# Performance work log

Hardware: AMD Instinct MI355X
Metric: run time of the kernel (lower is better)

Reference implementation:

```python
import jax, jax.numpy as jnp
import numpy as np
from jax import lax

L = 2048      # sentence length
V = 50000     # vocab size
E = 512       # embedding dim
HD = 512      # per-direction hidden (hidden_dim // 2)
H = 1024      # hidden_dim
T = 48        # tagset size
START, STOP = 46, 47
NEG = -10000.0


def setup_inputs() -> dict:
    key = jax.random.key(0)
    ks = iter(jax.random.split(key, 40))
    def n(shape, s=0.1):
        return jax.random.normal(next(ks), shape, dtype=jnp.float32) * s
    inp = {"sentence": jax.random.randint(next(ks), (L,), 0, V, dtype=jnp.int32)}
    inp["embedding"] = n((V, E), 1.0)
    for l, din in ((0, E), (1, H)):
        for d in ("", "r"):
            inp[f"w_ih_l{l}{d}"] = n((4 * HD, din))
            inp[f"w_hh_l{l}{d}"] = n((4 * HD, HD))
            inp[f"b_ih_l{l}{d}"] = n((4 * HD,))
            inp[f"b_hh_l{l}{d}"] = n((4 * HD,))
    inp["h0"] = n((4, HD), 1.0)
    inp["c0"] = n((4, HD), 1.0)
    inp["W_tag"] = n((T, H))
    inp["b_tag"] = n((T,))
    tr = n((T, T), 1.0)
    inp["transitions"] = tr.at[START, :].set(NEG).at[:, STOP].set(NEG)
    return inp


def _lstm_dir(x, w_ih, w_hh, b_ih, b_hh, h, c, reverse):
    # PyTorch LSTM cell, gates ordered (i, f, g, o). x: [L, Din]
    pre = x @ w_ih.T + (b_ih + b_hh)  # [L, 4*HD]
    def step(carry, p):
        h, c = carry
        g = p + h @ w_hh.T
        i, f, gg, o = jnp.split(g, 4)
        i, f, o = jax.nn.sigmoid(i), jax.nn.sigmoid(f), jax.nn.sigmoid(o)
        c = f * c + i * jnp.tanh(gg)
        h = o * jnp.tanh(c)
        return (h, c), h
    _, hs = lax.scan(step, (h, c), pre, reverse=reverse)
    return hs  # [L, HD], time-aligned with input


def _viterbi(feats, transitions):
    # max-plus recurrence over the tagset, vectorized per timestep
    init = jnp.full((T,), NEG, dtype=feats.dtype).at[START].set(0.0)
    def step(fv, feat):
        scores = fv[None, :] + transitions  # [next_tag, prev_tag]
        bp = jnp.argmax(scores, axis=1)
        return jnp.max(scores, axis=1) + feat, bp
    fv, bps = lax.scan(step, init, feats)  # bps: [L, T]
    terminal = fv + transitions[STOP]
    best = jnp.argmax(terminal)
    score = terminal[best]
    def back(tag, bp):
        prev = bp[tag]
        return prev, prev
    _, ys = lax.scan(back, best, bps, reverse=True)
    # ys[0] == START (dropped); path is tags for t = 0..L-1
    path = jnp.concatenate([ys[1:], best[None]])
    return score, path


def reference(sentence, embedding,
              w_ih_l0, w_hh_l0, b_ih_l0, b_hh_l0,
              w_ih_l0r, w_hh_l0r, b_ih_l0r, b_hh_l0r,
              w_ih_l1, w_hh_l1, b_ih_l1, b_hh_l1,
              w_ih_l1r, w_hh_l1r, b_ih_l1r, b_hh_l1r,
              h0, c0, W_tag, b_tag, transitions):
    embeds = embedding[sentence]  # [L, E]
    l0 = jnp.concatenate([
        _lstm_dir(embeds, w_ih_l0, w_hh_l0, b_ih_l0, b_hh_l0, h0[0], c0[0], False),
        _lstm_dir(embeds, w_ih_l0r, w_hh_l0r, b_ih_l0r, b_hh_l0r, h0[1], c0[1], True),
    ], axis=-1)  # [L, H]
    l1 = jnp.concatenate([
        _lstm_dir(l0, w_ih_l1, w_hh_l1, b_ih_l1, b_hh_l1, h0[2], c0[2], False),
        _lstm_dir(l0, w_ih_l1r, w_hh_l1r, b_ih_l1r, b_hh_l1r, h0[3], c0[3], True),
    ], axis=-1)  # [L, H]
    feats = l1 @ W_tag.T + b_tag  # [L, T]
    score, path = _viterbi(feats, transitions)
    return score, path
```

## Files before the change

kernel.cpp:

```cpp
#include <hip/hip_runtime.h>
#include <hip/hip_bf16.h>

#define L_SEQ 2048
#define HDIM 512
#define NGATE4 2048
#define TAGS 48
#define START_TAG 46
#define STOP_TAG 47
#define NWG 32
#define JPW 16

typedef float f32x4 __attribute__((ext_vector_type(4)));

#define BM 64
#define BN 64
#define BK 32
#define LDT 68

__global__ __launch_bounds__(256, 2)
void gemm_abt(const float* __restrict__ A, const float* __restrict__ B,
              const float* __restrict__ bias1, const float* __restrict__ bias2,
              float* __restrict__ C, int M, int N, int K,
              const int* __restrict__ gather)
{
  __shared__ float As[BK][LDT];
  __shared__ float Bs[BK][LDT];
  const int tid = threadIdx.x;
  const int m0 = blockIdx.x * BM;
  const int n0 = blockIdx.y * BN;
  const int tm = tid >> 4, tn = tid & 15;
  const int lr = tid >> 2, lk = (tid & 3) * 8;

  float acc[4][4];
#pragma unroll
  for (int i = 0; i < 4; ++i)
#pragma unroll
    for (int c = 0; c < 4; ++c) acc[i][c] = 0.f;

  const int am = m0 + lr;
  const float* arow = gather ? (A + (size_t)gather[am] * (size_t)K)
                             : (A + (size_t)am * (size_t)K);
  const int bn = n0 + lr;
  const float* brow = B + (size_t)bn * (size_t)K;
  const bool bok = (bn < N);

  for (int kt = 0; kt < K; kt += BK) {
    const float4 a0 = *(const float4*)(arow + kt + lk);
    const float4 a1 = *(const float4*)(arow + kt + lk + 4);
    float4 b0 = make_float4(0.f, 0.f, 0.f, 0.f);
    float4 b1 = make_float4(0.f, 0.f, 0.f, 0.f);
    if (bok) {
      b0 = *(const float4*)(brow + kt + lk);
      b1 = *(const float4*)(brow + kt + lk + 4);
    }
    As[lk + 0][lr] = a0.x; As[lk + 1][lr] = a0.y; As[lk + 2][lr] = a0.z; As[lk + 3][lr] = a0.w;
    As[lk + 4][lr] = a1.x; As[lk + 5][lr] = a1.y; As[lk + 6][lr] = a1.z; As[lk + 7][lr] = a1.w;
    Bs[lk + 0][lr] = b0.x; Bs[lk + 1][lr] = b0.y; Bs[lk + 2][lr] = b0.z; Bs[lk + 3][lr] = b0.w;
    Bs[lk + 4][lr] = b1.x; Bs[lk + 5][lr] = b1.y; Bs[lk + 6][lr] = b1.z; Bs[lk + 7][lr] = b1.w;
    __syncthreads();
#pragma unroll
    for (int kk = 0; kk < BK; ++kk) {
      const float4 av = *(const float4*)&As[kk][tm * 4];
      const float4 bv = *(const float4*)&Bs[kk][tn * 4];
      const float aa[4] = {av.x, av.y, av.z, av.w};
      const float bb[4] = {bv.x, bv.y, bv.z, bv.w};
#pragma unroll
      for (int i = 0; i < 4; ++i)
#pragma unroll
        for (int c = 0; c < 4; ++c)
          acc[i][c] += aa[i] * bb[c];
    }
    __syncthreads();
  }

  float bsum[4];
#pragma unroll
  for (int c = 0; c < 4; ++c) {
    const int n = n0 + tn * 4 + c;
    float bb = 0.f;
    if (n < N) { bb = bias1[n]; if (bias2) bb += bias2[n]; }
    bsum[c] = bb;
  }
#pragma unroll
  for (int i = 0; i < 4; ++i) {
    const int m = m0 + tm * 4 + i;
#pragma unroll
    for (int c = 0; c < 4; ++c) {
      const int n = n0 + tn * 4 + c;
      if (n < N) C[(size_t)m * N + n] = acc[i][c] + bsum[c];
    }
  }
}

__global__ __launch_bounds__(512, 1)
void lstm_layer(const float* __restrict__ pre_f, const float* __restrict__ pre_r,
                const float* __restrict__ whh_f, const float* __restrict__ whh_r,
                const float* __restrict__ h0, const float* __restrict__ c0,
                int hcrow_base,
                float* __restrict__ hs_out,
                unsigned long long* __restrict__ xch)
{
  const int sel = blockIdx.x & 7;
  if (sel > 1) return;
  const int dir = sel;
  const int wg  = blockIdx.x >> 3;
  const float* pre = dir ? pre_r : pre_f;
  const float* whh = dir ? whh_r : whh_f;
  const int tid = threadIdx.x;
  const int lane = tid & 63;
  const int wave = tid >> 6;
  const int q = lane & 15;
  const int g = lane >> 4;
  const int j0 = wg * JPW + wave * 2;
  const int hc = (hcrow_base + dir) * HDIM;
  const unsigned base = (unsigned)((hcrow_base >> 1) * 2048);

  __shared__ f32x4 wlds[8][2][8][64];
  __shared__ float h_lds[HDIM];

#pragma unroll
  for (int jj = 0; jj < 2; ++jj) {
    const float* wr = whh + (size_t)(g * HDIM + j0 + jj) * HDIM + 32 * q;
#pragma unroll
    for (int i = 0; i < 8; ++i)
      wlds[wave][jj][i][lane] = *(const f32x4*)(wr + 4 * ((i + q) & 7));
  }
  h_lds[tid] = h0[hc + tid];
  float cA = 0.f, cB = 0.f;
  if (lane == 0) { cA = c0[hc + j0]; cB = c0[hc + j0 + 1]; }
  __syncthreads();

  float pa = 0.f, pb = 0.f;
  if (q == 0) {
    const int t0 = dir ? (L_SEQ - 1) : 0;
    const float* pr = pre + (size_t)t0 * NGATE4 + g * HDIM + j0;
    pa = pr[0]; pb = pr[1];
  }

  for (int s = 0; s < L_SEQ; ++s) {
    const int t = dir ? (L_SEQ - 1 - s) : s;
    float pna = 0.f, pnb = 0.f;
    if (q == 0 && (s + 1 < L_SEQ)) {
      const int tnx = dir ? (L_SEQ - 2 - s) : (s + 1);
      const float* pr = pre + (size_t)tnx * NGATE4 + g * HDIM + j0;
      pna = pr[0]; pnb = pr[1];
    }

    f32x4 accA = {0.f, 0.f, 0.f, 0.f};
    f32x4 accB = {0.f, 0.f, 0.f, 0.f};
#pragma unroll
    for (int i = 0; i < 8; ++i) {
      const f32x4 hv = *(const f32x4*)&h_lds[32 * q + 4 * ((i + q) & 7)];
      accA += wlds[wave][0][i][lane] * hv;
      accB += wlds[wave][1][i][lane] * hv;
    }
    float aA = accA.x + accA.y + accA.z + accA.w;
    float aB = accB.x + accB.y + accB.z + accB.w;
#pragma unroll
    for (int m = 1; m < 16; m <<= 1) {
      aA += __shfl_xor(aA, m, 64);
      aB += __shfl_xor(aB, m, 64);
    }
    aA += pa; aB += pb;

    const float fA = __shfl(aA, 16, 64), gA = __shfl(aA, 32, 64), oA = __shfl(aA, 48, 64);
    const float fB = __shfl(aB, 16, 64), gB = __shfl(aB, 32, 64), oB = __shfl(aB, 48, 64);

    if (lane == 0) {
      const unsigned long long tag = (unsigned long long)(base + (unsigned)s + 1u);
      const size_t ob = (size_t)t * 1024 + dir * HDIM + j0;
      unsigned long long* xp = xch + ((s + 1) & 1) * 1024 + dir * HDIM + j0;
      {
        const float si = 1.f / (1.f + __expf(-aA));
        const float sf = 1.f / (1.f + __expf(-fA));
        const float tg = 1.f - 2.f / (__expf(2.f * gA) + 1.f);
        const float so = 1.f / (1.f + __expf(-oA));
        cA = sf * cA + si * tg;
        const float h = so * (1.f - 2.f / (__expf(2.f * cA) + 1.f));
        hs_out[ob] = h;
        const unsigned long long w =
            ((unsigned long long)__float_as_uint(h) << 32) | tag;
        __hip_atomic_store(xp, w, __ATOMIC_RELAXED, __HIP_MEMORY_SCOPE_AGENT);
      }
      {
        const float si = 1.f / (1.f + __expf(-aB));
        const float sf = 1.f / (1.f + __expf(-fB));
        const float tg = 1.f - 2.f / (__expf(2.f * gB) + 1.f);
        const float so = 1.f / (1.f + __expf(-oB));
        cB = sf * cB + si * tg;
        const float h = so * (1.f - 2.f / (__expf(2.f * cB) + 1.f));
        hs_out[ob + 1] = h;
        const unsigned long long w =
            ((unsigned long long)__float_as_uint(h) << 32) | tag;
        __hip_atomic_store(xp + 1, w, __ATOMIC_RELAXED, __HIP_MEMORY_SCOPE_AGENT);
      }
    }
    pa = pna; pb = pnb;

    if (s == L_SEQ - 1) break;

    __syncthreads();
    {
      const unsigned expect = base + (unsigned)s + 1u;
      const unsigned long long* wp = xch + ((s + 1) & 1) * 1024 + dir * HDIM + tid;
      unsigned long long v;
      do {
        v = __hip_atomic_load(wp, __ATOMIC_RELAXED, __HIP_MEMORY_SCOPE_AGENT);
      } while ((unsigned)v != expect);
      h_lds[tid] = __uint_as_float((unsigned)(v >> 32));
    }
    __syncthreads();
  }
}

__global__ __launch_bounds__(192, 1)
void viterbi_kernel(const float* __restrict__ feats,
                    const float* __restrict__ trans,
                    int* __restrict__ bp,
                    float* __restrict__ out)
{
  __shared__ float fv[TAGS];
  __shared__ float fvn[TAGS];
  const int tid = threadIdx.x;
  const int lane = tid & 63;
  const int wave = tid >> 6;
  const int q = lane & 3;
  const int j = wave * 16 + (lane >> 2);

  float trr[12];
#pragma unroll
  for (int kk = 0; kk < 12; ++kk) trr[kk] = trans[j * TAGS + q * 12 + kk];

  if (tid < TAGS) fv[tid] = (tid == START_TAG) ? 0.f : -10000.f;
  __syncthreads();

  for (int t = 0; t < L_SEQ; ++t) {
    const float ft = feats[t * TAGS + j];
    float best = -3.0e38f;
    int bi = 0;
#pragma unroll
    for (int kk = 0; kk < 12; ++kk) {
      const int k = q * 12 + kk;
      const float sc = fv[k] + trr[kk];
      if (sc > best) { best = sc; bi = k; }
    }
#pragma unroll
    for (int m = 1; m < 4; m <<= 1) {
      const float ov = __shfl_xor(best, m, 64);
      const int oi = __shfl_xor(bi, m, 64);
      if (ov > best || (ov == best && oi < bi)) { best = ov; bi = oi; }
    }
    __syncthreads();
    if (q == 0) {
      bp[t * TAGS + j] = bi;
      fv[j] = best + ft;
    }
    __syncthreads();
  }

  if (tid < TAGS) fvn[tid] = fv[tid] + trans[STOP_TAG * TAGS + tid];
  __syncthreads();
  if (tid == 0) {
    float best = -3.0e38f;
    int bi = 0;
    for (int k = 0; k < TAGS; ++k) {
      const float v = fvn[k];
      if (v > best) { best = v; bi = k; }
    }
    out[0] = best;
    int cur = bi;
    out[1 + (L_SEQ - 1)] = (float)cur;
    for (int t = L_SEQ - 2; t >= 0; --t) {
      cur = bp[(t + 1) * TAGS + cur];
      out[1 + t] = (float)cur;
    }
  }
}

extern "C" void kernel_launch(void* const* d_in, const int* in_sizes, int n_in,
                              void* d_out, int out_size, void* d_ws, size_t ws_size,
                              hipStream_t stream)
{
  const int*   sentence  = (const int*)  d_in[0];
  const float* embedding = (const float*)d_in[1];
  const float* w_ih_l0   = (const float*)d_in[2];
  const float* w_hh_l0   = (const float*)d_in[3];
  const float* b_ih_l0   = (const float*)d_in[4];
  const float* b_hh_l0   = (const float*)d_in[5];
  const float* w_ih_l0r  = (const float*)d_in[6];
  const float* w_hh_l0r  = (const float*)d_in[7];
  const float* b_ih_l0r  = (const float*)d_in[8];
  const float* b_hh_l0r  = (const float*)d_in[9];
  const float* w_ih_l1   = (const float*)d_in[10];
  const float* w_hh_l1   = (const float*)d_in[11];
  const float* b_ih_l1   = (const float*)d_in[12];
  const float* b_hh_l1   = (const float*)d_in[13];
  const float* w_ih_l1r  = (const float*)d_in[14];
  const float* w_hh_l1r  = (const float*)d_in[15];
  const float* b_ih_l1r  = (const float*)d_in[16];
  const float* b_hh_l1r  = (const float*)d_in[17];
  const float* h0        = (const float*)d_in[18];
  const float* c0        = (const float*)d_in[19];
  const float* W_tag     = (const float*)d_in[20];
  const float* b_tag     = (const float*)d_in[21];
  const float* trans     = (const float*)d_in[22];

  float* ws    = (float*)d_ws;
  float* pre_f = ws;
  float* pre_r = pre_f + (size_t)L_SEQ * NGATE4;
  float* l0out = pre_r + (size_t)L_SEQ * NGATE4;
  float* l1out = l0out + (size_t)L_SEQ * 1024;
  float* feats = l1out + (size_t)L_SEQ * 1024;
  unsigned long long* xch =
      (unsigned long long*)(feats + (size_t)L_SEQ * TAGS);
  int*   bp    = (int*)(xch + 2048);

  (void)hipMemsetAsync(xch, 0, 2048 * sizeof(unsigned long long), stream);

  dim3 blk(256);
  dim3 gfull(L_SEQ / BM, NGATE4 / BN);
  gemm_abt<<<gfull, blk, 0, stream>>>(embedding, w_ih_l0, b_ih_l0, b_hh_l0,
                                      pre_f, L_SEQ, NGATE4, 512, sentence);
  gemm_abt<<<gfull, blk, 0, stream>>>(embedding, w_ih_l0r, b_ih_l0r, b_hh_l0r,
                                      pre_r, L_SEQ, NGATE4, 512, sentence);
  lstm_layer<<<256, 512, 0, stream>>>(pre_f, pre_r, w_hh_l0, w_hh_l0r,
                                      h0, c0, 0, l0out, xch);
  gemm_abt<<<gfull, blk, 0, stream>>>(l0out, w_ih_l1, b_ih_l1, b_hh_l1,
                                      pre_f, L_SEQ, NGATE4, 1024, nullptr);
  gemm_abt<<<gfull, blk, 0, stream>>>(l0out, w_ih_l1r, b_ih_l1r, b_hh_l1r,
                                      pre_r, L_SEQ, NGATE4, 1024, nullptr);
  lstm_layer<<<256, 512, 0, stream>>>(pre_f, pre_r, w_hh_l1, w_hh_l1r,
                                      h0, c0, 2, l1out, xch);
  dim3 gfeat(L_SEQ / BM, 1);
  gemm_abt<<<gfeat, blk, 0, stream>>>(l1out, W_tag, b_tag, nullptr,
                                      feats, L_SEQ, TAGS, 1024, nullptr);
  viterbi_kernel<<<1, 192, 0, stream>>>(feats, trans, bp, (float*)d_out);
}
```

Measured before the change: 15.54 ms.

## Replicate hidden-state exchange buffer per workgroup to avoid polling contention

Each wave now computes the LSTM cell update redundantly in every lane and writes its new hidden values into 32 separate per-workgroup copies of the exchange buffer, one lane per destination workgroup. Each consumer workgroup then polls only its own private replica. The aim is to cut contention and cache-line sharing when all workgroups spin on the same global locations every timestep. In exchange, each step issues 32x more atomic stores and the exchange buffer becomes 32x larger.

```diff
diff --git a/kernel.cpp b/kernel.cpp
--- a/kernel.cpp
+++ b/kernel.cpp
@@ -126,8 +126,8 @@
       wlds[wave][jj][i][lane] = *(const f32x4*)(wr + 4 * ((i + q) & 7));
   }
   h_lds[tid] = h0[hc + tid];
-  float cA = 0.f, cB = 0.f;
-  if (lane == 0) { cA = c0[hc + j0]; cB = c0[hc + j0 + 1]; }
+  float cA = c0[hc + j0];
+  float cB = c0[hc + j0 + 1];
   __syncthreads();
 
   float pa = 0.f, pb = 0.f;
@@ -163,37 +163,41 @@
     }
     aA += pa; aB += pb;
 
-    const float fA = __shfl(aA, 16, 64), gA = __shfl(aA, 32, 64), oA = __shfl(aA, 48, 64);
-    const float fB = __shfl(aB, 16, 64), gB = __shfl(aB, 32, 64), oB = __shfl(aB, 48, 64);
-
-    if (lane == 0) {
-      const unsigned long long tag = (unsigned long long)(base + (unsigned)s + 1u);
-      const size_t ob = (size_t)t * 1024 + dir * HDIM + j0;
-      unsigned long long* xp = xch + ((s + 1) & 1) * 1024 + dir * HDIM + j0;
-      {
-        const float si = 1.f / (1.f + __expf(-aA));
-        const float sf = 1.f / (1.f + __expf(-fA));
-        const float tg = 1.f - 2.f / (__expf(2.f * gA) + 1.f);
-        const float so = 1.f / (1.f + __expf(-oA));
-        cA = sf * cA + si * tg;
-        const float h = so * (1.f - 2.f / (__expf(2.f * cA) + 1.f));
-        hs_out[ob] = h;
-        const unsigned long long w =
-            ((unsigned long long)__float_as_uint(h) << 32) | tag;
-        __hip_atomic_store(xp, w, __ATOMIC_RELAXED, __HIP_MEMORY_SCOPE_AGENT);
-      }
-      {
-        const float si = 1.f / (1.f + __expf(-aB));
-        const float sf = 1.f / (1.f + __expf(-fB));
-        const float tg = 1.f - 2.f / (__expf(2.f * gB) + 1.f);
-        const float so = 1.f / (1.f + __expf(-oB));
-        cB = sf * cB + si * tg;
-        const float h = so * (1.f - 2.f / (__expf(2.f * cB) + 1.f));
-        hs_out[ob + 1] = h;
-        const unsigned long long w =
-            ((unsigned long long)__float_as_uint(h) << 32) | tag;
-        __hip_atomic_store(xp + 1, w, __ATOMIC_RELAXED, __HIP_MEMORY_SCOPE_AGENT);
-      }
+    const float iA = __shfl(aA, 0, 64), fA = __shfl(aA, 16, 64);
+    const float gA = __shfl(aA, 32, 64), oA = __shfl(aA, 48, 64);
+    const float iB = __shfl(aB, 0, 64), fB = __shfl(aB, 16, 64);
+    const float gB = __shfl(aB, 32, 64), oB = __shfl(aB, 48, 64);
+
+    float hA, hB;
+    {
+      const float si = 1.f / (1.f + __expf(-iA));
+      const float sf = 1.f / (1.f + __expf(-fA));
+      const float tg = 1.f - 2.f / (__expf(2.f * gA) + 1.f);
+      const float so = 1.f / (1.f + __expf(-oA));
+      cA = sf * cA + si * tg;
+      hA = so * (1.f - 2.f / (__expf(2.f * cA) + 1.f));
+    }
+    {
+      const float si = 1.f / (1.f + __expf(-iB));
+      const float sf = 1.f / (1.f + __expf(-fB));
+      const float tg = 1.f - 2.f / (__expf(2.f * gB) + 1.f);
+      const float so = 1.f / (1.f + __expf(-oB));
+      cB = sf * cB + si * tg;
+      hB = so * (1.f - 2.f / (__expf(2.f * cB) + 1.f));
+    }
+
+    {
+      const int slot = (s + 1) & 1;
+      const float hv = (lane >= 32) ? hB : hA;
+      const unsigned long long w =
+          ((unsigned long long)__float_as_uint(hv) << 32)
+          | (unsigned long long)(base + (unsigned)s + 1u);
+      unsigned long long* xp = xch
+          + ((((size_t)(lane & 31)) * 2 + slot) * 2 + dir) * 512
+          + j0 + (lane >> 5);
+      __hip_atomic_store(xp, w, __ATOMIC_RELAXED, __HIP_MEMORY_SCOPE_AGENT);
+      if ((lane & 31) == 0)
+        hs_out[(size_t)t * 1024 + dir * HDIM + j0 + (lane >> 5)] = hv;
     }
     pa = pna; pb = pnb;
 
@@ -202,7 +206,8 @@
     __syncthreads();
     {
       const unsigned expect = base + (unsigned)s + 1u;
-      const unsigned long long* wp = xch + ((s + 1) & 1) * 1024 + dir * HDIM + tid;
+      const unsigned long long* wp = xch
+          + ((((size_t)wg) * 2 + ((s + 1) & 1)) * 2 + dir) * 512 + tid;
       unsigned long long v;
       do {
         v = __hip_atomic_load(wp, __ATOMIC_RELAXED, __HIP_MEMORY_SCOPE_AGENT);
@@ -313,9 +318,9 @@
   float* feats = l1out + (size_t)L_SEQ * 1024;
   unsigned long long* xch =
       (unsigned long long*)(feats + (size_t)L_SEQ * TAGS);
-  int*   bp    = (int*)(xch + 2048);
-
-  (void)hipMemsetAsync(xch, 0, 2048 * sizeof(unsigned long long), stream);
+  int*   bp    = (int*)(xch + (size_t)NWG * 2 * 2 * 512);
+
+  (void)hipMemsetAsync(xch, 0, (size_t)NWG * 2 * 2 * 512 * sizeof(unsigned long long), stream);
 
   dim3 blk(256);
   dim3 gfull(L_SEQ / BM, NGATE4 / BN);
```

After: 19.43 ms. +25.1%, slower.

## Split LSTM hidden-state exchange into fast plain-store and slow atomic fallback buffers

Applied to the files above, without the earlier changes.

The per-step hidden-state exchange between workgroups now writes each pair of tagged h values twice. One copy is a single vectorized non-atomic 128-bit store to a fast buffer, which is polled with a raw global_load using the sc0 cache bit. The other copy goes out as agent-scope atomics to a slow buffer, which is checked every 16 polls as a fallback. The aim is to cut cross-workgroup synchronization latency in the sequential recurrence. The cost is extra stores and reliance on cache-coherence behaviour of the plain path, with the fallback guarding against stale reads.

```diff
diff --git a/kernel.cpp b/kernel.cpp
--- a/kernel.cpp
+++ b/kernel.cpp
@@ -98,7 +98,8 @@
                 const float* __restrict__ h0, const float* __restrict__ c0,
                 int hcrow_base,
                 float* __restrict__ hs_out,
-                unsigned long long* __restrict__ xch)
+                unsigned long long* __restrict__ xch_fast,
+                unsigned long long* __restrict__ xch_slow)
 {
   const int sel = blockIdx.x & 7;
   if (sel > 1) return;
@@ -168,19 +169,15 @@
 
     if (lane == 0) {
       const unsigned long long tag = (unsigned long long)(base + (unsigned)s + 1u);
-      const size_t ob = (size_t)t * 1024 + dir * HDIM + j0;
-      unsigned long long* xp = xch + ((s + 1) & 1) * 1024 + dir * HDIM + j0;
+      const size_t wb = ((size_t)((s + 1) & 1) * 2 + dir) * 512 + j0;
+      float hA, hB;
       {
         const float si = 1.f / (1.f + __expf(-aA));
         const float sf = 1.f / (1.f + __expf(-fA));
         const float tg = 1.f - 2.f / (__expf(2.f * gA) + 1.f);
         const float so = 1.f / (1.f + __expf(-oA));
         cA = sf * cA + si * tg;
-        const float h = so * (1.f - 2.f / (__expf(2.f * cA) + 1.f));
-        hs_out[ob] = h;
-        const unsigned long long w =
-            ((unsigned long long)__float_as_uint(h) << 32) | tag;
-        __hip_atomic_store(xp, w, __ATOMIC_RELAXED, __HIP_MEMORY_SCOPE_AGENT);
+        hA = so * (1.f - 2.f / (__expf(2.f * cA) + 1.f));
       }
       {
         const float si = 1.f / (1.f + __expf(-aB));
@@ -188,12 +185,18 @@
         const float tg = 1.f - 2.f / (__expf(2.f * gB) + 1.f);
         const float so = 1.f / (1.f + __expf(-oB));
         cB = sf * cB + si * tg;
-        const float h = so * (1.f - 2.f / (__expf(2.f * cB) + 1.f));
-        hs_out[ob + 1] = h;
-        const unsigned long long w =
-            ((unsigned long long)__float_as_uint(h) << 32) | tag;
-        __hip_atomic_store(xp + 1, w, __ATOMIC_RELAXED, __HIP_MEMORY_SCOPE_AGENT);
+        hB = so * (1.f - 2.f / (__expf(2.f * cB) + 1.f));
       }
+      const unsigned long long wA =
+          ((unsigned long long)__float_as_uint(hA) << 32) | tag;
+      const unsigned long long wB =
+          ((unsigned long long)__float_as_uint(hB) << 32) | tag;
+      ulonglong2 pk; pk.x = wA; pk.y = wB;
+      *(ulonglong2*)(xch_fast + wb) = pk;
+      __hip_atomic_store(xch_slow + wb, wA, __ATOMIC_RELAXED, __HIP_MEMORY_SCOPE_AGENT);
+      __hip_atomic_store(xch_slow + wb + 1, wB, __ATOMIC_RELAXED, __HIP_MEMORY_SCOPE_AGENT);
+      float2 hv2; hv2.x = hA; hv2.y = hB;
+      *(float2*)&hs_out[(size_t)t * 1024 + dir * HDIM + j0] = hv2;
     }
     pa = pna; pb = pnb;
 
@@ -202,11 +205,21 @@
     __syncthreads();
     {
       const unsigned expect = base + (unsigned)s + 1u;
-      const unsigned long long* wp = xch + ((s + 1) & 1) * 1024 + dir * HDIM + tid;
+      const size_t wi = ((size_t)((s + 1) & 1) * 2 + dir) * 512 + tid;
+      const unsigned long long* fp = xch_fast + wi;
       unsigned long long v;
-      do {
-        v = __hip_atomic_load(wp, __ATOMIC_RELAXED, __HIP_MEMORY_SCOPE_AGENT);
-      } while ((unsigned)v != expect);
+      int it = 0;
+      for (;;) {
+        asm volatile("global_load_dwordx2 %0, %1, off sc0\n\t"
+                     "s_waitcnt vmcnt(0)"
+                     : "=v"(v) : "v"(fp) : "memory");
+        if ((unsigned)v == expect) break;
+        if ((++it & 15) == 0) {
+          v = __hip_atomic_load(xch_slow + wi, __ATOMIC_RELAXED,
+                                __HIP_MEMORY_SCOPE_AGENT);
+          if ((unsigned)v == expect) break;
+        }
+      }
       h_lds[tid] = __uint_as_float((unsigned)(v >> 32));
     }
     __syncthreads();
@@ -311,11 +324,12 @@
   float* l0out = pre_r + (size_t)L_SEQ * NGATE4;
   float* l1out = l0out + (size_t)L_SEQ * 1024;
   float* feats = l1out + (size_t)L_SEQ * 1024;
-  unsigned long long* xch =
+  unsigned long long* xch_fast =
       (unsigned long long*)(feats + (size_t)L_SEQ * TAGS);
-  int*   bp    = (int*)(xch + 2048);
-
-  (void)hipMemsetAsync(xch, 0, 2048 * sizeof(unsigned long long), stream);
+  unsigned long long* xch_slow = xch_fast + 2048;
+  int*   bp    = (int*)(xch_slow + 2048);
+
+  (void)hipMemsetAsync(xch_fast, 0, 2 * 2048 * sizeof(unsigned long long), stream);
 
   dim3 blk(256);
   dim3 gfull(L_SEQ / BM, NGATE4 / BN);
@@ -324,13 +338,13 @@
   gemm_abt<<<gfull, blk, 0, stream>>>(embedding, w_ih_l0r, b_ih_l0r, b_hh_l0r,
                                       pre_r, L_SEQ, NGATE4, 512, sentence);
   lstm_layer<<<256, 512, 0, stream>>>(pre_f, pre_r, w_hh_l0, w_hh_l0r,
-                                      h0, c0, 0, l0out, xch);
+                                      h0, c0, 0, l0out, xch_fast, xch_slow);
   gemm_abt<<<gfull, blk, 0, stream>>>(l0out, w_ih_l1, b_ih_l1, b_hh_l1,
                                       pre_f, L_SEQ, NGATE4, 1024, nullptr);
   gemm_abt<<<gfull, blk, 0, stream>>>(l0out, w_ih_l1r, b_ih_l1r, b_hh_l1r,
                                       pre_r, L_SEQ, NGATE4, 1024, nullptr);
   lstm_layer<<<256, 512, 0, stream>>>(pre_f, pre_r, w_hh_l1, w_hh_l1r,
-                                      h0, c0, 2, l1out, xch);
+                                      h0, c0, 2, l1out, xch_fast, xch_slow);
   dim3 gfeat(L_SEQ / BM, 1);
   gemm_abt<<<gfeat, blk, 0, stream>>>(l1out, W_tag, b_tag, nullptr,
                                       feats, L_SEQ, TAGS, 1024, nullptr);
```

Measured after the change: 19.18 ms. 1.23x slower.
